# Performance work log

Measured on AMD Instinct MI355X. Metric: run time of the kernel, lower is better.

The kernel has to match this reference:

```python
import jax, jax.numpy as jnp
import numpy as np

N = 100000      # nodes
E = 800000      # edges
F_IN = 256      # input feature dim
HID = 256       # hidden_channels
H = 8           # heads
C = HID // H    # per-head dim = 32
OUT = 128       # out_channels
EPS_BN = 1e-5
NEG_SLOPE = 0.2


def _segment_softmax(logits, seg, n):
    # logits: [E, H], softmax over edges sharing the same destination node
    m = jax.ops.segment_max(logits, seg, num_segments=n)          # [N, H]
    m = jnp.where(jnp.isfinite(m), m, 0.0)                         # nodes with no in-edges
    ex = jnp.exp(logits - m[seg])                                  # [E, H]
    denom = jax.ops.segment_sum(ex, seg, num_segments=n)          # [N, H]
    return ex / (denom[seg] + 1e-16)


def _gatv2_layer(x, src, dst, Wl, bl, Wr, br, att, bias):
    # PyG GATv2Conv (eval, concat=True): lin_l on source, lin_r on target
    n = x.shape[0]
    xl = (x @ Wl + bl).reshape(n, H, C)   # [N, H, C]
    xr = (x @ Wr + br).reshape(n, H, C)   # [N, H, C]
    e = jax.nn.leaky_relu(xl[src] + xr[dst], NEG_SLOPE)            # [E, H, C]
    logits = jnp.einsum('ehc,hc->eh', e, att)                      # [E, H]
    alpha = _segment_softmax(logits, dst, n)                       # [E, H]
    msg = xl[src] * alpha[:, :, None]                              # [E, H, C]
    out = jax.ops.segment_sum(msg, dst, num_segments=n)            # [N, H, C]
    return out.reshape(n, H * C) + bias


def _batchnorm(x, gamma, beta):
    # training-mode batch statistics (deterministic), biased variance
    mu = x.mean(axis=0)
    var = x.var(axis=0)
    return gamma * (x - mu) * jax.lax.rsqrt(var + EPS_BN) + beta


def setup_inputs() -> dict:
    key = jax.random.key(0)
    ks = jax.random.split(key, 12)
    s = 0.05
    z = jnp.zeros
    o = jnp.ones
    rn = lambda k, shp: jax.random.normal(k, shp, jnp.float32) * s
    return {
        'x': jax.random.normal(ks[0], (N, F_IN), jnp.float32),
        'edge_index': jax.random.randint(ks[1], (2, E), 0, N, jnp.int32),
        'Wl1': rn(ks[2], (F_IN, HID)), 'bl1': z((HID,), jnp.float32),
        'Wr1': rn(ks[3], (F_IN, HID)), 'br1': z((HID,), jnp.float32),
        'att1': rn(ks[4], (H, C)), 'bias1': z((HID,), jnp.float32),
        'gamma1': o((HID,), jnp.float32), 'beta1': z((HID,), jnp.float32),
        'Wl2': rn(ks[5], (HID, HID)), 'bl2': z((HID,), jnp.float32),
        'Wr2': rn(ks[6], (HID, HID)), 'br2': z((HID,), jnp.float32),
        'att2': rn(ks[7], (H, C)), 'bias2': z((HID,), jnp.float32),
        'gamma2': o((HID,), jnp.float32), 'beta2': z((HID,), jnp.float32),
        'Wfc': rn(ks[8], (HID, OUT)), 'bfc': z((OUT,), jnp.float32),
    }


def reference(x, edge_index, Wl1, bl1, Wr1, br1, att1, bias1, gamma1, beta1,
              Wl2, bl2, Wr2, br2, att2, bias2, gamma2, beta2, Wfc, bfc):
    src, dst = edge_index[0], edge_index[1]
    h = _gatv2_layer(x, src, dst, Wl1, bl1, Wr1, br1, att1, bias1)
    h = jax.nn.elu(_batchnorm(h, gamma1, beta1))
    h = _gatv2_layer(h, src, dst, Wl2, bl2, Wr2, br2, att2, bias2)
    h = jax.nn.elu(_batchnorm(h, gamma2, beta2))
    h = h @ Wfc + bfc
    # F.normalize(p=2, dim=-1)
    norm = jnp.maximum(jnp.linalg.norm(h, axis=-1, keepdims=True), 1e-12)
    return h / norm
```

## Files before the change

kernel.cpp:

```cpp
#include <hip/hip_runtime.h>
#include <math.h>

#define N_NODES 100000
#define N_EDGES 800000
#define NPAD    100096
#define FDIM 256
#define HEADS 8
#define CDIM 32
#define OUTF 128

#define SCAN_BLOCK 256
#define SCAN_NBLK ((N_NODES + SCAN_BLOCK - 1) / SCAN_BLOCK)

typedef _Float16 f16x2 __attribute__((ext_vector_type(2)));
typedef _Float16 f16x8 __attribute__((ext_vector_type(8)));
typedef float  f32x4 __attribute__((ext_vector_type(4)));
typedef unsigned short u16;

__device__ __forceinline__ u16 f2h(float f) {
    union { _Float16 h; u16 u; } c;
    c.h = (_Float16)f;
    return c.u;
}
__device__ __forceinline__ float h2f(u16 u) {
    union { u16 u; _Float16 h; } c;
    c.u = u;
    return (float)c.h;
}
__device__ __forceinline__ f16x2 u2h2(unsigned u) {
    return __builtin_bit_cast(f16x2, u);
}

__device__ __forceinline__ void gload_lds16(const void* g, void* l) {
    __builtin_amdgcn_global_load_lds((const __attribute__((address_space(1))) void*)g,
                                     (__attribute__((address_space(3))) void*)l, 16, 0, 0);
}

__global__ void cast_half(const float* __restrict__ src, int n_valid4, int n_pad4,
                          u16* __restrict__ dst) {
    int i = blockIdx.x * blockDim.x + threadIdx.x;
    int stride = gridDim.x * blockDim.x;
    for (; i < n_pad4; i += stride) {
        f32x4 v = {0.f, 0.f, 0.f, 0.f};
        if (i < n_valid4) v = ((const f32x4*)src)[i];
        ((ushort4*)dst)[i] = make_ushort4(f2h(v[0]), f2h(v[1]), f2h(v[2]), f2h(v[3]));
    }
}

__global__ void prep_w_layer(const float* __restrict__ Wl, const float* __restrict__ Wr,
                             u16* __restrict__ Wt) {
    int idx = blockIdx.x * blockDim.x + threadIdx.x;
    if (idx >= 512 * 256) return;
    int n = idx >> 8, k = idx & 255;
    float w = (n < 256) ? Wl[k * 256 + n] : Wr[k * 256 + (n - 256)];
    Wt[idx] = f2h(w);
}

__global__ void prep_w_fc(const float* __restrict__ Wfc, u16* __restrict__ Wt) {
    int idx = blockIdx.x * blockDim.x + threadIdx.x;
    if (idx >= 128 * 256) return;
    int n = idx >> 8, k = idx & 255;
    Wt[idx] = f2h(Wfc[k * 128 + n]);
}

template <bool HOUT>
__global__ __launch_bounds__(256) void gemm_h(
        const u16* __restrict__ A, const u16* __restrict__ Wt,
        const float* __restrict__ bias0, const float* __restrict__ bias1,
        void* __restrict__ C0v, void* __restrict__ C1v, int ldc, int M) {
    __shared__ __align__(16) u16 lA[128 * 64];
    __shared__ __align__(16) u16 lB[128 * 64];

    int tid = threadIdx.x;
    int wid = tid >> 6, lane = tid & 63;
    int wm = wid >> 1, wn = wid & 1;
    int m0 = blockIdx.x * 128, n0 = blockIdx.y * 128;
    int lr = lane & 15, lk = lane >> 4;

    f32x4 acc[4][4] = {};

#pragma unroll 1
    for (int k0 = 0; k0 < 256; k0 += 64) {
#pragma unroll
        for (int i = 0; i < 4; i++) {
            int t = i * 256 + tid;
            int row = t >> 3;
            int ch = (t & 7) ^ (row & 7);
            gload_lds16(A + (size_t)(m0 + row) * 256 + k0 + ch * 8,
                        (char*)lA + i * 4096 + wid * 1024);
        }
#pragma unroll
        for (int i = 0; i < 4; i++) {
            int t = i * 256 + tid;
            int row = t >> 3;
            int ch = (t & 7) ^ (row & 7);
            gload_lds16(Wt + (size_t)(n0 + row) * 256 + k0 + ch * 8,
                        (char*)lB + i * 4096 + wid * 1024);
        }
        __syncthreads();

#pragma unroll
        for (int kk = 0; kk < 2; kk++) {
            f16x8 af[4], bf[4];
#pragma unroll
            for (int mr = 0; mr < 4; mr++) {
                int r = wm * 64 + mr * 16 + lr;
                int q = (kk * 4 + lk) ^ (r & 7);
                af[mr] = *(const f16x8*)&lA[r * 64 + q * 8];
            }
#pragma unroll
            for (int nr = 0; nr < 4; nr++) {
                int r = wn * 64 + nr * 16 + lr;
                int q = (kk * 4 + lk) ^ (r & 7);
                bf[nr] = *(const f16x8*)&lB[r * 64 + q * 8];
            }
#pragma unroll
            for (int mr = 0; mr < 4; mr++)
#pragma unroll
                for (int nr = 0; nr < 4; nr++)
                    acc[mr][nr] = __builtin_amdgcn_mfma_f32_16x16x32_f16(
                        af[mr], bf[nr], acc[mr][nr], 0, 0, 0);
        }
        __syncthreads();
    }

#pragma unroll
    for (int mr = 0; mr < 4; mr++) {
#pragma unroll
        for (int nr = 0; nr < 4; nr++) {
            int col = n0 + wn * 64 + nr * 16 + lr;
            void* Cp; const float* bp; int c;
            if (col < 256) { Cp = C0v; bp = bias0; c = col; }
            else           { Cp = C1v; bp = bias1; c = col - 256; }
            float b = bp[c];
#pragma unroll
            for (int j = 0; j < 4; j++) {
                int row = m0 + wm * 64 + mr * 16 + lk * 4 + j;
                if (row < M) {
                    float v = acc[mr][nr][j] + b;
                    if constexpr (HOUT)
                        ((u16*)Cp)[(size_t)row * ldc + c] = f2h(v);
                    else
                        ((float*)Cp)[(size_t)row * ldc + c] = v;
                }
            }
        }
    }
}

__global__ void count_deg(const int* __restrict__ dstA, int* __restrict__ deg) {
    int i = blockIdx.x * blockDim.x + threadIdx.x;
    int stride = gridDim.x * blockDim.x;
    for (; i < N_EDGES; i += stride) atomicAdd(&deg[dstA[i]], 1);
}

__global__ void scan_phase1(const int* __restrict__ deg, int* __restrict__ blocksum) {
    __shared__ int sdata[SCAN_BLOCK];
    int i = blockIdx.x * SCAN_BLOCK + threadIdx.x;
    sdata[threadIdx.x] = (i < N_NODES) ? deg[i] : 0;
    __syncthreads();
    for (int off = SCAN_BLOCK / 2; off > 0; off >>= 1) {
        if (threadIdx.x < off) sdata[threadIdx.x] += sdata[threadIdx.x + off];
        __syncthreads();
    }
    if (threadIdx.x == 0) blocksum[blockIdx.x] = sdata[0];
}

__global__ void scan_phase2(int* __restrict__ blocksum) {
    __shared__ int part[512];
    int t = threadIdx.x;
    int v = (t < SCAN_NBLK) ? blocksum[t] : 0;
    part[t] = v;
    __syncthreads();
    for (int off = 1; off < 512; off <<= 1) {
        int u = 0;
        if (t >= off) u = part[t - off];
        __syncthreads();
        if (t >= off) part[t] += u;
        __syncthreads();
    }
    if (t < SCAN_NBLK) blocksum[t] = part[t] - v;
}

__global__ void scan_phase3(const int* __restrict__ deg, const int* __restrict__ blockoff,
                            int* __restrict__ rowstart, int* __restrict__ cursor) {
    __shared__ int part[SCAN_BLOCK];
    int t = threadIdx.x;
    int i = blockIdx.x * SCAN_BLOCK + t;
    int v = (i < N_NODES) ? deg[i] : 0;
    part[t] = v;
    __syncthreads();
    for (int off = 1; off < SCAN_BLOCK; off <<= 1) {
        int u = 0;
        if (t >= off) u = part[t - off];
        __syncthreads();
        if (t >= off) part[t] += u;
        __syncthreads();
    }
    if (i < N_NODES) {
        int excl = blockoff[blockIdx.x] + part[t] - v;
        rowstart[i] = excl;
        cursor[i] = excl;
        if (i == N_NODES - 1) rowstart[N_NODES] = blockoff[blockIdx.x] + part[t];
    }
}

__global__ void fill_csr(const int* __restrict__ srcA, const int* __restrict__ dstA,
                         int* __restrict__ cursor, int* __restrict__ csr_src) {
    int i = blockIdx.x * blockDim.x + threadIdx.x;
    int stride = gridDim.x * blockDim.x;
    for (; i < N_EDGES; i += stride) {
        int pos = atomicAdd(&cursor[dstA[i]], 1);
        csr_src[pos] = srcA[i];
    }
}

__global__ void gat_fused(const u16* __restrict__ xl, const u16* __restrict__ xr,
                          const int* __restrict__ rowstart, const int* __restrict__ csr_src,
                          const float* __restrict__ att, u16* __restrict__ out) {
    int wid = (blockIdx.x * blockDim.x + threadIdx.x) >> 6;
    int lane = threadIdx.x & 63;
    if (wid >= N_NODES) return;
    int hl = lane & 31;
    int up = lane >> 5;
    int c0 = hl * 8;

    uint4 xru = *(const uint4*)(xr + (size_t)wid * FDIM + c0);
    f16x2 xr0 = u2h2(xru.x), xr1 = u2h2(xru.y), xr2 = u2h2(xru.z), xr3 = u2h2(xru.w);
    f32x4 av0 = *(const f32x4*)(att + c0);
    f32x4 av1 = *(const f32x4*)(att + c0 + 4);
    f16x2 a0 = {(_Float16)av0[0], (_Float16)av0[1]};
    f16x2 a1 = {(_Float16)av0[2], (_Float16)av0[3]};
    f16x2 a2 = {(_Float16)av1[0], (_Float16)av1[1]};
    f16x2 a3 = {(_Float16)av1[2], (_Float16)av1[3]};
    const f16x2 k02 = {(_Float16)0.2f, (_Float16)0.2f};

    float acc[8] = {0.f, 0.f, 0.f, 0.f, 0.f, 0.f, 0.f, 0.f};
    float den = 0.f;

    int jb = rowstart[wid], je = rowstart[wid + 1];
    if (jb < je) {
        int jlast = je - 1;
        int nsteps = (je - jb + 1) >> 1;
        int i0 = jb + up;     if (i0 > jlast) i0 = jlast;
        uint4 u0 = *(const uint4*)(xl + (size_t)csr_src[i0] * FDIM + c0);
        int i1 = jb + 2 + up; if (i1 > jlast) i1 = jlast;
        uint4 u1 = *(const uint4*)(xl + (size_t)csr_src[i1] * FDIM + c0);

        for (int t = 0; t < nsteps; ++t) {
            int in_ = jb + 2 * t + 4 + up; if (in_ > jlast) in_ = jlast;
            uint4 un = *(const uint4*)(xl + (size_t)csr_src[in_] * FDIM + c0);

            int myidx = jb + 2 * t + up;
            f16x2 x0 = u2h2(u0.x), x1 = u2h2(u0.y), x2 = u2h2(u0.z), x3 = u2h2(u0.w);
            f16x2 v0 = x0 + xr0, v1 = x1 + xr1, v2 = x2 + xr2, v3 = x3 + xr3;
            f16x2 t0 = __builtin_elementwise_max(v0, v0 * k02);
            f16x2 t1 = __builtin_elementwise_max(v1, v1 * k02);
            f16x2 t2 = __builtin_elementwise_max(v2, v2 * k02);
            f16x2 t3 = __builtin_elementwise_max(v3, v3 * k02);
            float s = __builtin_amdgcn_fdot2(t0, a0, 0.f, false);
            s = __builtin_amdgcn_fdot2(t1, a1, s, false);
            s = __builtin_amdgcn_fdot2(t2, a2, s, false);
            s = __builtin_amdgcn_fdot2(t3, a3, s, false);
            s += __shfl_xor(s, 1);
            s += __shfl_xor(s, 2);
            float e = (myidx <= jlast) ? __expf(s) : 0.f;
            den += e;
            acc[0] += e * (float)x0[0]; acc[1] += e * (float)x0[1];
            acc[2] += e * (float)x1[0]; acc[3] += e * (float)x1[1];
            acc[4] += e * (float)x2[0]; acc[5] += e * (float)x2[1];
            acc[6] += e * (float)x3[0]; acc[7] += e * (float)x3[1];
            u0 = u1; u1 = un;
        }
    }
    den += __shfl_xor(den, 32);
#pragma unroll
    for (int i = 0; i < 8; i++) acc[i] += __shfl_xor(acc[i], 32);

    if (up == 0) {
        float inv = 1.f / (den + 1e-16f);
        u16 h[8];
#pragma unroll
        for (int i = 0; i < 8; i++) h[i] = f2h(acc[i] * inv);
        *(uint4*)(out + (size_t)wid * FDIM + c0) = *(const uint4*)h;
    }
}

__global__ void bn_stats_h(const u16* __restrict__ X, float* __restrict__ sum,
                           float* __restrict__ sumsq, int nrows) {
    int col = threadIdx.x;
    float s = 0.f, ss = 0.f;
    for (int r = blockIdx.x; r < nrows; r += gridDim.x) {
        float v = h2f(X[(size_t)r * FDIM + col]);
        s += v;
        ss += v * v;
    }
    atomicAdd(&sum[col], s);
    atomicAdd(&sumsq[col], ss);
}

__global__ void bn_finalize(const float* __restrict__ sum, const float* __restrict__ sumsq,
                            const float* __restrict__ gamma, const float* __restrict__ beta,
                            float* __restrict__ scale, float* __restrict__ shift) {
    int c = threadIdx.x;
    float mean = sum[c] * (1.f / N_NODES);
    float var = sumsq[c] * (1.f / N_NODES) - mean * mean;
    float sc = gamma[c] * rsqrtf(var + 1e-5f);
    scale[c] = sc;
    shift[c] = beta[c] - mean * sc;
}

__global__ void bn_elu_h(const u16* __restrict__ X, const float* __restrict__ scale,
                         const float* __restrict__ shift, u16* __restrict__ dst) {
    int i = blockIdx.x * blockDim.x + threadIdx.x;
    int stride = gridDim.x * blockDim.x;
    const int n_valid4 = N_NODES * FDIM / 4;
    const int n_pad4 = NPAD * FDIM / 4;
    for (; i < n_pad4; i += stride) {
        u16 h[4] = {0, 0, 0, 0};
        if (i < n_valid4) {
            ushort4 v = ((const ushort4*)X)[i];
            int c0 = (i * 4) & (FDIM - 1);
            float f0 = h2f(v.x) * scale[c0 + 0] + shift[c0 + 0];
            float f1 = h2f(v.y) * scale[c0 + 1] + shift[c0 + 1];
            float f2 = h2f(v.z) * scale[c0 + 2] + shift[c0 + 2];
            float f3 = h2f(v.w) * scale[c0 + 3] + shift[c0 + 3];
            f0 = f0 > 0.f ? f0 : expf(f0) - 1.f;
            f1 = f1 > 0.f ? f1 : expf(f1) - 1.f;
            f2 = f2 > 0.f ? f2 : expf(f2) - 1.f;
            f3 = f3 > 0.f ? f3 : expf(f3) - 1.f;
            h[0] = f2h(f0); h[1] = f2h(f1); h[2] = f2h(f2); h[3] = f2h(f3);
        }
        ((ushort4*)dst)[i] = make_ushort4(h[0], h[1], h[2], h[3]);
    }
}

__global__ void l2norm(float* __restrict__ Y, int nrows) {
    int gtid = blockIdx.x * blockDim.x + threadIdx.x;
    int wave = gtid >> 6;
    int lane = threadIdx.x & 63;
    int nwaves = (gridDim.x * blockDim.x) >> 6;
    for (int r = wave; r < nrows; r += nwaves) {
        float v0 = Y[(size_t)r * OUTF + lane];
        float v1 = Y[(size_t)r * OUTF + 64 + lane];
        float ss = v0 * v0 + v1 * v1;
        ss += __shfl_xor(ss, 32);
        ss += __shfl_xor(ss, 16);
        ss += __shfl_xor(ss, 8);
        ss += __shfl_xor(ss, 4);
        ss += __shfl_xor(ss, 2);
        ss += __shfl_xor(ss, 1);
        float inv = 1.f / fmaxf(sqrtf(ss), 1e-12f);
        Y[(size_t)r * OUTF + lane] = v0 * inv;
        Y[(size_t)r * OUTF + 64 + lane] = v1 * inv;
    }
}

extern "C" void kernel_launch(void* const* d_in, const int* in_sizes, int n_in,
                              void* d_out, int out_size, void* d_ws, size_t ws_size,
                              hipStream_t stream) {
    const float* x     = (const float*)d_in[0];
    const int*   ei    = (const int*)d_in[1];
    const float* Wl1   = (const float*)d_in[2];
    const float* bl1   = (const float*)d_in[3];
    const float* Wr1   = (const float*)d_in[4];
    const float* br1   = (const float*)d_in[5];
    const float* att1  = (const float*)d_in[6];
    const float* gamma1 = (const float*)d_in[8];
    const float* beta1  = (const float*)d_in[9];
    const float* Wl2   = (const float*)d_in[10];
    const float* bl2   = (const float*)d_in[11];
    const float* Wr2   = (const float*)d_in[12];
    const float* br2   = (const float*)d_in[13];
    const float* att2  = (const float*)d_in[14];
    const float* gamma2 = (const float*)d_in[16];
    const float* beta2  = (const float*)d_in[17];
    const float* Wfc   = (const float*)d_in[18];
    const float* bfc   = (const float*)d_in[19];

    const int* srcA = ei;
    const int* dstA = ei + N_EDGES;

    const size_t REG = (size_t)NPAD * FDIM * 4;
    char* p = (char*)d_ws;
    char* R0 = p;            p += REG;
    char* R1 = p;            p += REG;
    char* R2 = p;            p += REG;
    u16* WTH   = (u16*)p;              p += 512 * 256 * 2;
    float* SUM = (float*)p;            p += FDIM * 4;
    float* SQ  = (float*)p;            p += FDIM * 4;
    float* SC  = (float*)p;            p += FDIM * 4;
    float* SH  = (float*)p;            p += FDIM * 4;
    int* DEG      = (int*)p;           p += (size_t)N_NODES * 4;
    int* ROWSTART = (int*)p;           p += (size_t)(N_NODES + 1) * 4;
    int* CURSOR   = (int*)p;           p += (size_t)N_NODES * 4;
    int* CSR      = (int*)p;           p += (size_t)N_EDGES * 4;
    int* BLKSUM   = (int*)p;           p += (size_t)SCAN_NBLK * 4;

    const int gat_grid = (N_NODES + 3) / 4;
    const dim3 gemm_grid_layer(NPAD / 128, 4);
    const dim3 gemm_grid_fc(NPAD / 128, 1);

    hipMemsetAsync(DEG, 0, (size_t)N_NODES * sizeof(int), stream);
    count_deg<<<2048, 256, 0, stream>>>(dstA, DEG);
    scan_phase1<<<SCAN_NBLK, SCAN_BLOCK, 0, stream>>>(DEG, BLKSUM);
    scan_phase2<<<1, 512, 0, stream>>>(BLKSUM);
    scan_phase3<<<SCAN_NBLK, SCAN_BLOCK, 0, stream>>>(DEG, BLKSUM, ROWSTART, CURSOR);
    fill_csr<<<2048, 256, 0, stream>>>(srcA, dstA, CURSOR, CSR);

    cast_half<<<4096, 256, 0, stream>>>(x, N_NODES * FDIM / 4, NPAD * FDIM / 4, (u16*)R0);
    prep_w_layer<<<512, 256, 0, stream>>>(Wl1, Wr1, WTH);
    gemm_h<true><<<gemm_grid_layer, 256, 0, stream>>>((u16*)R0, WTH, bl1, br1, R1, R2, 256, N_NODES);
    gat_fused<<<gat_grid, 256, 0, stream>>>((u16*)R1, (u16*)R2, ROWSTART, CSR, att1, (u16*)R0);

    hipMemsetAsync(SUM, 0, 2 * FDIM * sizeof(float), stream);
    bn_stats_h<<<1024, 256, 0, stream>>>((u16*)R0, SUM, SQ, N_NODES);
    bn_finalize<<<1, 256, 0, stream>>>(SUM, SQ, gamma1, beta1, SC, SH);
    bn_elu_h<<<2048, 256, 0, stream>>>((u16*)R0, SC, SH, (u16*)R1);

    prep_w_layer<<<512, 256, 0, stream>>>(Wl2, Wr2, WTH);
    gemm_h<true><<<gemm_grid_layer, 256, 0, stream>>>((u16*)R1, WTH, bl2, br2, R2, R0, 256, N_NODES);
    gat_fused<<<gat_grid, 256, 0, stream>>>((u16*)R2, (u16*)R0, ROWSTART, CSR, att2, (u16*)R1);

    hipMemsetAsync(SUM, 0, 2 * FDIM * sizeof(float), stream);
    bn_stats_h<<<1024, 256, 0, stream>>>((u16*)R1, SUM, SQ, N_NODES);
    bn_finalize<<<1, 256, 0, stream>>>(SUM, SQ, gamma2, beta2, SC, SH);
    bn_elu_h<<<2048, 256, 0, stream>>>((u16*)R1, SC, SH, (u16*)R2);

    prep_w_fc<<<128, 256, 0, stream>>>(Wfc, WTH);
    gemm_h<false><<<gemm_grid_fc, 256, 0, stream>>>((u16*)R2, WTH, bfc, bfc, d_out, d_out, 128, N_NODES);
    l2norm<<<2048, 256, 0, stream>>>((float*)d_out, N_NODES);
}
```

Baseline: 658.6 us.

## Replace LDS-tiled GEMM with register-resident weights streaming A rows

The shared-memory tiled GEMM is replaced by a kernel where each wave keeps its 32-column slice of the weight matrix in registers for all K, then loops over 16 row tiles of A loaded straight from global memory. This removes LDS staging and block barriers. The cost is that all four waves in a block reload the same A rows, relying on cache, and register pressure rises, which may lower occupancy. Bias selection also moves to a per-block choice.

```diff
diff --git a/kernel.cpp b/kernel.cpp
--- a/kernel.cpp
+++ b/kernel.cpp
@@ -9,6 +9,10 @@
 #define CDIM 32
 #define OUTF 128
 
+#define MTILES_TOTAL (NPAD / 16)
+#define MT_PER_BLOCK 16
+#define GEMM_GX (MTILES_TOTAL / MT_PER_BLOCK)
+
 #define SCAN_BLOCK 256
 #define SCAN_NBLK ((N_NODES + SCAN_BLOCK - 1) / SCAN_BLOCK)
 
@@ -29,11 +33,6 @@
 }
 __device__ __forceinline__ f16x2 u2h2(unsigned u) {
     return __builtin_bit_cast(f16x2, u);
-}
-
-__device__ __forceinline__ void gload_lds16(const void* g, void* l) {
-    __builtin_amdgcn_global_load_lds((const __attribute__((address_space(1))) void*)g,
-                                     (__attribute__((address_space(3))) void*)l, 16, 0, 0);
 }
 
 __global__ void cast_half(const float* __restrict__ src, int n_valid4, int n_pad4,
@@ -64,84 +63,57 @@
 }
 
 template <bool HOUT>
-__global__ __launch_bounds__(256) void gemm_h(
+__global__ __launch_bounds__(256) void gemm_s(
         const u16* __restrict__ A, const u16* __restrict__ Wt,
         const float* __restrict__ bias0, const float* __restrict__ bias1,
         void* __restrict__ C0v, void* __restrict__ C1v, int ldc, int M) {
-    __shared__ __align__(16) u16 lA[128 * 64];
-    __shared__ __align__(16) u16 lB[128 * 64];
-
     int tid = threadIdx.x;
-    int wid = tid >> 6, lane = tid & 63;
-    int wm = wid >> 1, wn = wid & 1;
-    int m0 = blockIdx.x * 128, n0 = blockIdx.y * 128;
+    int w = tid >> 6, lane = tid & 63;
     int lr = lane & 15, lk = lane >> 4;
 
-    f32x4 acc[4][4] = {};
-
-#pragma unroll 1
-    for (int k0 = 0; k0 < 256; k0 += 64) {
-#pragma unroll
-        for (int i = 0; i < 4; i++) {
-            int t = i * 256 + tid;
-            int row = t >> 3;
-            int ch = (t & 7) ^ (row & 7);
-            gload_lds16(A + (size_t)(m0 + row) * 256 + k0 + ch * 8,
-                        (char*)lA + i * 4096 + wid * 1024);
+    int ngl = blockIdx.y * 128 + w * 32;
+
+    f16x8 b[2][8];
+#pragma unroll
+    for (int nr = 0; nr < 2; nr++)
+#pragma unroll
+        for (int ks = 0; ks < 8; ks++)
+            b[nr][ks] = *(const f16x8*)&Wt[(size_t)(ngl + nr * 16 + lr) * 256 + ks * 32 + lk * 8];
+
+    const float* bp; char* Cp; int cbase;
+    if (blockIdx.y < 2) { bp = bias0; Cp = (char*)C0v; cbase = blockIdx.y * 128; }
+    else                { bp = bias1; Cp = (char*)C1v; cbase = (blockIdx.y - 2) * 128; }
+    int colw = cbase + w * 32;
+    float bias[2] = {bp[colw + lr], bp[colw + 16 + lr]};
+
+    int mt0 = blockIdx.x * MT_PER_BLOCK;
+#pragma unroll 2
+    for (int t = 0; t < MT_PER_BLOCK; ++t) {
+        int row0 = (mt0 + t) * 16;
+        f16x8 a[8];
+#pragma unroll
+        for (int ks = 0; ks < 8; ks++)
+            a[ks] = *(const f16x8*)&A[(size_t)(row0 + lr) * 256 + ks * 32 + lk * 8];
+
+        f32x4 acc[2] = {};
+#pragma unroll
+        for (int ks = 0; ks < 8; ks++) {
+            acc[0] = __builtin_amdgcn_mfma_f32_16x16x32_f16(a[ks], b[0][ks], acc[0], 0, 0, 0);
+            acc[1] = __builtin_amdgcn_mfma_f32_16x16x32_f16(a[ks], b[1][ks], acc[1], 0, 0, 0);
         }
-#pragma unroll
-        for (int i = 0; i < 4; i++) {
-            int t = i * 256 + tid;
-            int row = t >> 3;
-            int ch = (t & 7) ^ (row & 7);
-            gload_lds16(Wt + (size_t)(n0 + row) * 256 + k0 + ch * 8,
-                        (char*)lB + i * 4096 + wid * 1024);
-        }
-        __syncthreads();
-
-#pragma unroll
-        for (int kk = 0; kk < 2; kk++) {
-            f16x8 af[4], bf[4];
-#pragma unroll
-            for (int mr = 0; mr < 4; mr++) {
-                int r = wm * 64 + mr * 16 + lr;
-                int q = (kk * 4 + lk) ^ (r & 7);
-                af[mr] = *(const f16x8*)&lA[r * 64 + q * 8];
-            }
-#pragma unroll
-            for (int nr = 0; nr < 4; nr++) {
-                int r = wn * 64 + nr * 16 + lr;
-                int q = (kk * 4 + lk) ^ (r & 7);
-                bf[nr] = *(const f16x8*)&lB[r * 64 + q * 8];
-            }
-#pragma unroll
-            for (int mr = 0; mr < 4; mr++)
-#pragma unroll
-                for (int nr = 0; nr < 4; nr++)
-                    acc[mr][nr] = __builtin_amdgcn_mfma_f32_16x16x32_f16(
-                        af[mr], bf[nr], acc[mr][nr], 0, 0, 0);
-        }
-        __syncthreads();
-    }
-
-#pragma unroll
-    for (int mr = 0; mr < 4; mr++) {
-#pragma unroll
-        for (int nr = 0; nr < 4; nr++) {
-            int col = n0 + wn * 64 + nr * 16 + lr;
-            void* Cp; const float* bp; int c;
-            if (col < 256) { Cp = C0v; bp = bias0; c = col; }
-            else           { Cp = C1v; bp = bias1; c = col - 256; }
-            float b = bp[c];
+
+#pragma unroll
+        for (int nr = 0; nr < 2; nr++) {
+            int col = colw + nr * 16 + lr;
 #pragma unroll
             for (int j = 0; j < 4; j++) {
-                int row = m0 + wm * 64 + mr * 16 + lk * 4 + j;
+                int row = row0 + lk * 4 + j;
                 if (row < M) {
-                    float v = acc[mr][nr][j] + b;
+                    float v = acc[nr][j] + bias[nr];
                     if constexpr (HOUT)
-                        ((u16*)Cp)[(size_t)row * ldc + c] = f2h(v);
+                        ((u16*)Cp)[(size_t)row * ldc + col] = f2h(v);
                     else
-                        ((float*)Cp)[(size_t)row * ldc + c] = v;
+                        ((float*)Cp)[(size_t)row * ldc + col] = v;
                 }
             }
         }
@@ -398,8 +370,8 @@
     int* BLKSUM   = (int*)p;           p += (size_t)SCAN_NBLK * 4;
 
     const int gat_grid = (N_NODES + 3) / 4;
-    const dim3 gemm_grid_layer(NPAD / 128, 4);
-    const dim3 gemm_grid_fc(NPAD / 128, 1);
+    const dim3 gemm_grid_layer(GEMM_GX, 4);
+    const dim3 gemm_grid_fc(GEMM_GX, 1);
 
     hipMemsetAsync(DEG, 0, (size_t)N_NODES * sizeof(int), stream);
     count_deg<<<2048, 256, 0, stream>>>(dstA, DEG);
@@ -410,7 +382,7 @@
 
     cast_half<<<4096, 256, 0, stream>>>(x, N_NODES * FDIM / 4, NPAD * FDIM / 4, (u16*)R0);
     prep_w_layer<<<512, 256, 0, stream>>>(Wl1, Wr1, WTH);
-    gemm_h<true><<<gemm_grid_layer, 256, 0, stream>>>((u16*)R0, WTH, bl1, br1, R1, R2, 256, N_NODES);
+    gemm_s<true><<<gemm_grid_layer, 256, 0, stream>>>((u16*)R0, WTH, bl1, br1, R1, R2, 256, N_NODES);
     gat_fused<<<gat_grid, 256, 0, stream>>>((u16*)R1, (u16*)R2, ROWSTART, CSR, att1, (u16*)R0);
 
     hipMemsetAsync(SUM, 0, 2 * FDIM * sizeof(float), stream);
@@ -419,7 +391,7 @@
     bn_elu_h<<<2048, 256, 0, stream>>>((u16*)R0, SC, SH, (u16*)R1);
 
     prep_w_layer<<<512, 256, 0, stream>>>(Wl2, Wr2, WTH);
-    gemm_h<true><<<gemm_grid_layer, 256, 0, stream>>>((u16*)R1, WTH, bl2, br2, R2, R0, 256, N_NODES);
+    gemm_s<true><<<gemm_grid_layer, 256, 0, stream>>>((u16*)R1, WTH, bl2, br2, R2, R0, 256, N_NODES);
     gat_fused<<<gat_grid, 256, 0, stream>>>((u16*)R2, (u16*)R0, ROWSTART, CSR, att2, (u16*)R1);
 
     hipMemsetAsync(SUM, 0, 2 * FDIM * sizeof(float), stream);
@@ -428,6 +400,6 @@
     bn_elu_h<<<2048, 256, 0, stream>>>((u16*)R1, SC, SH, (u16*)R2);
 
     prep_w_fc<<<128, 256, 0, stream>>>(Wfc, WTH);
-    gemm_h<false><<<gemm_grid_fc, 256, 0, stream>>>((u16*)R2, WTH, bfc, bfc, d_out, d_out, 128, N_NODES);
+    gemm_s<false><<<gemm_grid_fc, 256, 0, stream>>>((u16*)R2, WTH, bfc, bfc, d_out, d_out, 128, N_NODES);
     l2norm<<<2048, 256, 0, stream>>>((float*)d_out, N_NODES);
 }
```

After: 737.4 us. 1.12x slower.
